# Optimization experiments

Measured on AMD Instinct MI355X. Metric: run time of the kernel, lower is better.

The kernel has to match this reference:

```python
import jax, jax.numpy as jnp
import numpy as np

B, T, W, D = 16, 32, 128, 1024  # batch, turns, words/turn, hidden dim


def setup_inputs() -> dict:
    key = jax.random.key(0)
    ks = jax.random.split(key, 6)
    source = jax.random.normal(ks[0], (B, 1, D), dtype=jnp.float32)
    memory_bank = jax.random.normal(ks[1], (B, T, W, D), dtype=jnp.float32)
    # lengths in [1, W] so no turn is fully masked (matches real padded batches)
    memory_lengths = jax.random.randint(ks[2], (B, T), 1, W + 1)
    memory_turns = jax.random.randint(ks[3], (B,), 1, T + 1)
    # nn.Linear(indim, outdim, bias=False): y = x @ W^T; store as [indim, outdim]
    W_word = jax.random.normal(ks[4], (D, D), dtype=jnp.float32) * 0.02
    W_turn = jax.random.normal(ks[5], (D, D), dtype=jnp.float32) * 0.02
    return {"source": source, "memory_bank": memory_bank,
            "memory_lengths": memory_lengths, "memory_turns": memory_turns,
            "W_word": W_word, "W_turn": W_turn}


def reference(source, memory_bank, memory_lengths, memory_turns, W_word, W_turn):
    # source: [B,1,D]; memory_bank: [B,T,W,D]; target_l == 1
    b, t, w, d = memory_bank.shape
    # ---- word-level attention (per turn) ----
    q_w = source @ W_word                                   # [B,1,D]
    word_scores = jnp.einsum('bqd,btwd->btw', q_w, memory_bank)  # [B,T,W]
    word_mask = jnp.arange(w)[None, None, :] < memory_lengths[:, :, None]
    word_scores = jnp.where(word_mask, word_scores, -jnp.inf)
    word_attn = jax.nn.softmax(word_scores, axis=-1)        # [B,T,W]
    # zero out fully-padded turns (length == 0)
    word_attn = word_attn * (memory_lengths > 0)[:, :, None].astype(word_attn.dtype)
    cw = jnp.einsum('btw,btwd->btd', word_attn, memory_bank)  # [B,T,D]
    # ---- turn-level attention ----
    q_t = source @ W_turn                                   # [B,1,D]
    turn_scores = jnp.einsum('bqd,btd->bt', q_t, cw)        # [B,T]
    turn_mask = jnp.arange(t)[None, :] < memory_turns[:, None]
    turn_scores = jnp.where(turn_mask, turn_scores, -jnp.inf)
    turn_attn = jax.nn.softmax(turn_scores, axis=-1)        # [B,T]
    ct = jnp.einsum('bt,btd->bd', turn_attn, cw)            # [B,D]
    return ct
```

## Files before the change

kernel.cpp:

```cpp
#include <hip/hip_runtime.h>
#include <math.h>

#define Bn 16
#define Tn 32
#define Wn 128
#define Dn 1024


__global__ __launch_bounds__(256) void qproj_kernel(
    const float* __restrict__ src, const float* __restrict__ Ww,
    const float* __restrict__ Wt, float* __restrict__ qwp, float* __restrict__ qtp)
{
    __shared__ float s_lds[16 * 132];
    const int tid = threadIdx.x;
    const int mat = blockIdx.x >> 7;
    const int chunk = (blockIdx.x >> 3) & 15;
    const int isl = blockIdx.x & 7;

    #pragma unroll
    for (int k = 0; k < 8; ++k) {
        int idx = k * 256 + tid;
        int bb = idx >> 7, ii = idx & 127;
        s_lds[bb * 132 + ii] = src[bb * Dn + isl * 128 + ii];
    }
    __syncthreads();

    const int lane = tid & 63, wv = tid >> 6;
    const int col4 = chunk * 16 + (lane & 15);
    const int b = (lane >> 4) + 4 * wv;
    const float4* W4 = (const float4*)(mat ? Wt : Ww);
    const float* sb = s_lds + b * 132;

    float4 acc = make_float4(0.f, 0.f, 0.f, 0.f);
    #pragma unroll 8
    for (int ii = 0; ii < 128; ++ii) {
        float4 w4 = W4[(size_t)(isl * 128 + ii) * 256 + col4];
        float s = sb[ii];
        acc.x = fmaf(s, w4.x, acc.x);
        acc.y = fmaf(s, w4.y, acc.y);
        acc.z = fmaf(s, w4.z, acc.z);
        acc.w = fmaf(s, w4.w, acc.w);
    }
    float* qo = (mat ? qtp : qwp) + isl * (Bn * Dn);
    ((float4*)(qo + b * Dn))[col4] = acc;
}

__global__ __launch_bounds__(256) void qreduce_kernel(
    const float* __restrict__ qwp, const float* __restrict__ qtp,
    float* __restrict__ qw, float* __restrict__ qt)
{
    const int blk = blockIdx.x;
    const float4* in4 = (const float4*)((blk & 16) ? qtp : qwp);
    float4* out4 = (float4*)((blk & 16) ? qt : qw);
    const int idx = (blk & 15) * 256 + threadIdx.x;
    float4 a = make_float4(0.f, 0.f, 0.f, 0.f);
    #pragma unroll
    for (int s = 0; s < 8; ++s) {
        float4 v = in4[s * 4096 + idx];
        a.x += v.x; a.y += v.y; a.z += v.z; a.w += v.w;
    }
    out4[idx] = a;
}

__global__ __launch_bounds__(1024) void word_attn_kernel(
    const float* __restrict__ mem, const float* __restrict__ qw,
    const float* __restrict__ qt, const int* __restrict__ lens,
    const int* __restrict__ turns, float* __restrict__ cw, float* __restrict__ ts)
{
    const int bt = blockIdx.x;
    const int b = bt >> 5, t = bt & 31;
    if (t >= turns[b]) return;
    const int len = lens[bt];

    const int tid = threadIdx.x, lane = tid & 63, wv = tid >> 6;
    const float* rowb = mem + (size_t)bt * (Wn * Dn);

    const float4* qa = (const float4*)(qw + b * Dn);
    float4 q[4];
    #pragma unroll
    for (int c = 0; c < 4; ++c) q[c] = qa[c * 64 + lane];

    float m = -INFINITY, l = 0.f;
    float4 acc[4];
    #pragma unroll
    for (int c = 0; c < 4; ++c) acc[c] = make_float4(0.f, 0.f, 0.f, 0.f);

    for (int w = wv; w < len; w += 16) {
        const float4* r4 = (const float4*)(rowb + (size_t)w * Dn);
        float4 x[4];
        #pragma unroll
        for (int c = 0; c < 4; ++c) x[c] = r4[c * 64 + lane];
        float s = 0.f;
        #pragma unroll
        for (int c = 0; c < 4; ++c) {
            s = fmaf(q[c].x, x[c].x, s);
            s = fmaf(q[c].y, x[c].y, s);
            s = fmaf(q[c].z, x[c].z, s);
            s = fmaf(q[c].w, x[c].w, s);
        }
        #pragma unroll
        for (int off = 32; off >= 1; off >>= 1) s += __shfl_xor(s, off, 64);

        float mn = fmaxf(m, s);
        float sc = (m == -INFINITY) ? 0.f : __expf(m - mn);
        float p = __expf(s - mn);
        l = l * sc + p;
        #pragma unroll
        for (int c = 0; c < 4; ++c) {
            acc[c].x = fmaf(acc[c].x, sc, p * x[c].x);
            acc[c].y = fmaf(acc[c].y, sc, p * x[c].y);
            acc[c].z = fmaf(acc[c].z, sc, p * x[c].z);
            acc[c].w = fmaf(acc[c].w, sc, p * x[c].w);
        }
        m = mn;
    }

    __shared__ float m_s[16], l_s[16], red[16];
    __shared__ float acc_s[16 * 1024];
    if (lane == 0) { m_s[wv] = m; l_s[wv] = l; }
    float4* as4 = (float4*)(acc_s + wv * 1024);
    #pragma unroll
    for (int c = 0; c < 4; ++c) as4[c * 64 + lane] = acc[c];
    __syncthreads();

    float M = -INFINITY;
    #pragma unroll
    for (int v = 0; v < 16; ++v) M = fmaxf(M, m_s[v]);
    float L = 0.f, cacc = 0.f;
    #pragma unroll
    for (int v = 0; v < 16; ++v) {
        float f = (l_s[v] > 0.f) ? __expf(m_s[v] - M) : 0.f;
        L += f * l_s[v];
        cacc = fmaf(f, acc_s[v * 1024 + tid], cacc);
    }
    cacc *= 1.f / L;
    cw[(size_t)bt * Dn + tid] = cacc;

    float p = qt[b * Dn + tid] * cacc;
    #pragma unroll
    for (int off = 32; off >= 1; off >>= 1) p += __shfl_xor(p, off, 64);
    if (lane == 0) red[wv] = p;
    __syncthreads();
    if (tid == 0) {
        float r = 0.f;
        #pragma unroll
        for (int v = 0; v < 16; ++v) r += red[v];
        ts[bt] = r;
    }
}

__global__ __launch_bounds__(256) void turn_attn_kernel(
    const float* __restrict__ cw, const float* __restrict__ ts,
    const int* __restrict__ turns, float* __restrict__ out)
{
    const int b = blockIdx.x;
    const int n = turns[b];
    const int tid = threadIdx.x;
    __shared__ float attn[32];
    if (tid < 32) {
        float s = (tid < n) ? ts[b * Tn + tid] : -INFINITY;
        float mm = s;
        #pragma unroll
        for (int off = 16; off >= 1; off >>= 1) mm = fmaxf(mm, __shfl_xor(mm, off, 32));
        float e = (tid < n) ? __expf(s - mm) : 0.f;
        float sum = e;
        #pragma unroll
        for (int off = 16; off >= 1; off >>= 1) sum += __shfl_xor(sum, off, 32);
        attn[tid] = e / sum;
    }
    __syncthreads();
    float4 a = make_float4(0.f, 0.f, 0.f, 0.f);
    for (int tt = 0; tt < n; ++tt) {
        float wgt = attn[tt];
        float4 c = ((const float4*)(cw + ((size_t)b * Tn + tt) * Dn))[tid];
        a.x = fmaf(wgt, c.x, a.x);
        a.y = fmaf(wgt, c.y, a.y);
        a.z = fmaf(wgt, c.z, a.z);
        a.w = fmaf(wgt, c.w, a.w);
    }
    ((float4*)(out + b * Dn))[tid] = a;
}

extern "C" void kernel_launch(void* const* d_in, const int* in_sizes, int n_in,
                              void* d_out, int out_size, void* d_ws, size_t ws_size,
                              hipStream_t stream) {
    (void)in_sizes; (void)n_in; (void)out_size; (void)ws_size;
    const float* src   = (const float*)d_in[0];
    const float* mem   = (const float*)d_in[1];
    const int*   lens  = (const int*)d_in[2];
    const int*   turns = (const int*)d_in[3];
    const float* Ww    = (const float*)d_in[4];
    const float* Wt    = (const float*)d_in[5];
    float* ws  = (float*)d_ws;
    float* qwp = ws;
    float* qtp = ws + 8 * Bn * Dn;
    float* qw  = ws + 16 * Bn * Dn;
    float* qt  = ws + 17 * Bn * Dn;
    float* cw  = ws + 18 * Bn * Dn;
    float* ts  = cw + (size_t)Bn * Tn * Dn;
    float* out = (float*)d_out;

    hipLaunchKernelGGL(qproj_kernel, dim3(256), dim3(256), 0, stream,
                       src, Ww, Wt, qwp, qtp);
    hipLaunchKernelGGL(qreduce_kernel, dim3(32), dim3(256), 0, stream,
                       qwp, qtp, qw, qt);
    hipLaunchKernelGGL(word_attn_kernel, dim3(Bn * Tn), dim3(1024), 0, stream,
                       mem, qw, qt, lens, turns, cw, ts);
    hipLaunchKernelGGL(turn_attn_kernel, dim3(Bn), dim3(256), 0, stream,
                       cw, ts, turns, out);
}
```

Before: 351.8 us.

## Replace q partial-sum reduce kernel with atomics and prefetch next memory row

The split-K query projection now accumulates its partial sums straight into a zeroed buffer with float atomic adds. This removes the separate reduce kernel and the partial-sum workspace, at the cost of an extra memset and atomic traffic. The word attention loop is software-pipelined: the next row's float4 loads are issued before the current row is processed, to hide global memory latency, at the cost of more registers per thread. Atomic accumulation makes the float summation order nondeterministic.

After: 355.8 us. Within noise of the previous version (+1.1%).

```diff
diff --git a/kernel.cpp b/kernel.cpp
--- a/kernel.cpp
+++ b/kernel.cpp
@@ -9,7 +9,7 @@
 
 __global__ __launch_bounds__(256) void qproj_kernel(
     const float* __restrict__ src, const float* __restrict__ Ww,
-    const float* __restrict__ Wt, float* __restrict__ qwp, float* __restrict__ qtp)
+    const float* __restrict__ Wt, float* __restrict__ q)
 {
     __shared__ float s_lds[16 * 132];
     const int tid = threadIdx.x;
@@ -41,31 +41,17 @@
         acc.z = fmaf(s, w4.z, acc.z);
         acc.w = fmaf(s, w4.w, acc.w);
     }
-    float* qo = (mat ? qtp : qwp) + isl * (Bn * Dn);
-    ((float4*)(qo + b * Dn))[col4] = acc;
-}
-
-__global__ __launch_bounds__(256) void qreduce_kernel(
-    const float* __restrict__ qwp, const float* __restrict__ qtp,
-    float* __restrict__ qw, float* __restrict__ qt)
-{
-    const int blk = blockIdx.x;
-    const float4* in4 = (const float4*)((blk & 16) ? qtp : qwp);
-    float4* out4 = (float4*)((blk & 16) ? qt : qw);
-    const int idx = (blk & 15) * 256 + threadIdx.x;
-    float4 a = make_float4(0.f, 0.f, 0.f, 0.f);
-    #pragma unroll
-    for (int s = 0; s < 8; ++s) {
-        float4 v = in4[s * 4096 + idx];
-        a.x += v.x; a.y += v.y; a.z += v.z; a.w += v.w;
-    }
-    out4[idx] = a;
+    float* dst = q + (size_t)mat * (Bn * Dn) + b * Dn + col4 * 4;
+    unsafeAtomicAdd(dst + 0, acc.x);
+    unsafeAtomicAdd(dst + 1, acc.y);
+    unsafeAtomicAdd(dst + 2, acc.z);
+    unsafeAtomicAdd(dst + 3, acc.w);
 }
 
 __global__ __launch_bounds__(1024) void word_attn_kernel(
-    const float* __restrict__ mem, const float* __restrict__ qw,
-    const float* __restrict__ qt, const int* __restrict__ lens,
-    const int* __restrict__ turns, float* __restrict__ cw, float* __restrict__ ts)
+    const float* __restrict__ mem, const float* __restrict__ q,
+    const int* __restrict__ lens, const int* __restrict__ turns,
+    float* __restrict__ cw, float* __restrict__ ts)
 {
     const int bt = blockIdx.x;
     const int b = bt >> 5, t = bt & 31;
@@ -75,28 +61,38 @@
     const int tid = threadIdx.x, lane = tid & 63, wv = tid >> 6;
     const float* rowb = mem + (size_t)bt * (Wn * Dn);
 
-    const float4* qa = (const float4*)(qw + b * Dn);
-    float4 q[4];
-    #pragma unroll
-    for (int c = 0; c < 4; ++c) q[c] = qa[c * 64 + lane];
+    const float4* qa = (const float4*)(q + b * Dn);
+    float4 qf[4];
+    #pragma unroll
+    for (int c = 0; c < 4; ++c) qf[c] = qa[c * 64 + lane];
 
     float m = -INFINITY, l = 0.f;
     float4 acc[4];
     #pragma unroll
     for (int c = 0; c < 4; ++c) acc[c] = make_float4(0.f, 0.f, 0.f, 0.f);
 
-    for (int w = wv; w < len; w += 16) {
+    int w = wv;
+    float4 x[4];
+    if (w < len) {
         const float4* r4 = (const float4*)(rowb + (size_t)w * Dn);
-        float4 x[4];
         #pragma unroll
         for (int c = 0; c < 4; ++c) x[c] = r4[c * 64 + lane];
+    }
+    while (w < len) {
+        const int wn = w + 16;
+        float4 xn[4];
+        if (wn < len) {
+            const float4* r4 = (const float4*)(rowb + (size_t)wn * Dn);
+            #pragma unroll
+            for (int c = 0; c < 4; ++c) xn[c] = r4[c * 64 + lane];
+        }
         float s = 0.f;
         #pragma unroll
         for (int c = 0; c < 4; ++c) {
-            s = fmaf(q[c].x, x[c].x, s);
-            s = fmaf(q[c].y, x[c].y, s);
-            s = fmaf(q[c].z, x[c].z, s);
-            s = fmaf(q[c].w, x[c].w, s);
+            s = fmaf(qf[c].x, x[c].x, s);
+            s = fmaf(qf[c].y, x[c].y, s);
+            s = fmaf(qf[c].z, x[c].z, s);
+            s = fmaf(qf[c].w, x[c].w, s);
         }
         #pragma unroll
         for (int off = 32; off >= 1; off >>= 1) s += __shfl_xor(s, off, 64);
@@ -113,6 +109,9 @@
             acc[c].w = fmaf(acc[c].w, sc, p * x[c].w);
         }
         m = mn;
+        #pragma unroll
+        for (int c = 0; c < 4; ++c) x[c] = xn[c];
+        w = wn;
     }
 
     __shared__ float m_s[16], l_s[16], red[16];
@@ -136,7 +135,7 @@
     cacc *= 1.f / L;
     cw[(size_t)bt * Dn + tid] = cacc;
 
-    float p = qt[b * Dn + tid] * cacc;
+    float p = q[Bn * Dn + b * Dn + tid] * cacc;
     #pragma unroll
     for (int off = 32; off >= 1; off >>= 1) p += __shfl_xor(p, off, 64);
     if (lane == 0) red[wv] = p;
@@ -191,21 +190,17 @@
     const int*   turns = (const int*)d_in[3];
     const float* Ww    = (const float*)d_in[4];
     const float* Wt    = (const float*)d_in[5];
-    float* ws  = (float*)d_ws;
-    float* qwp = ws;
-    float* qtp = ws + 8 * Bn * Dn;
-    float* qw  = ws + 16 * Bn * Dn;
-    float* qt  = ws + 17 * Bn * Dn;
-    float* cw  = ws + 18 * Bn * Dn;
-    float* ts  = cw + (size_t)Bn * Tn * Dn;
+    float* ws = (float*)d_ws;
+    float* q  = ws;
+    float* cw = ws + 2 * Bn * Dn;
+    float* ts = cw + (size_t)Bn * Tn * Dn;
     float* out = (float*)d_out;
 
+    hipMemsetAsync(q, 0, 2 * Bn * Dn * sizeof(float), stream);
     hipLaunchKernelGGL(qproj_kernel, dim3(256), dim3(256), 0, stream,
-                       src, Ww, Wt, qwp, qtp);
-    hipLaunchKernelGGL(qreduce_kernel, dim3(32), dim3(256), 0, stream,
-                       qwp, qtp, qw, qt);
+                       src, Ww, Wt, q);
     hipLaunchKernelGGL(word_attn_kernel, dim3(Bn * Tn), dim3(1024), 0, stream,
-                       mem, qw, qt, lens, turns, cw, ts);
+                       mem, q, lens, turns, cw, ts);
     hipLaunchKernelGGL(turn_attn_kernel, dim3(Bn), dim3(256), 0, stream,
                        cw, ts, turns, out);
 }
```
